# Performance work log

Hardware: AMD Instinct MI355X
Metric: run time of the kernel (lower is better)

Reference implementation:

```python
import jax, jax.numpy as jnp
import numpy as np

NA, NM = 200000, 100000
DA, DM = 128, 64
H = 128
E = 1000000


def _lin(x, W, b):
    # torch nn.Linear: y = x @ W.T + b, W: [out, in]
    return x @ W.T + b


def setup_inputs() -> dict:
    key = jax.random.key(0)
    ks = jax.random.split(key, 24)
    s = 0.02
    inp = {
        "x_account": jax.random.normal(ks[0], (NA, DA), jnp.float32),
        "x_merchant": jax.random.normal(ks[1], (NM, DM), jnp.float32),
        "e_am_src": jax.random.randint(ks[2], (E,), 0, NA, jnp.int32),
        "e_am_dst": jax.random.randint(ks[3], (E,), 0, NM, jnp.int32),
        "e_am_w": jax.random.uniform(ks[4], (E,), jnp.float32),
        "e_ma_src": jax.random.randint(ks[5], (E,), 0, NM, jnp.int32),
        "e_ma_dst": jax.random.randint(ks[6], (E,), 0, NA, jnp.int32),
        "e_ma_w": jax.random.uniform(ks[7], (E,), jnp.float32),
        # type_proj
        "Wp_a": s * jax.random.normal(ks[8], (H, DA), jnp.float32),
        "bp_a": jnp.zeros((H,), jnp.float32),
        "Wp_m": s * jax.random.normal(ks[9], (H, DM), jnp.float32),
        "bp_m": jnp.zeros((H,), jnp.float32),
        # rel_linears: account->merchant:txn (in=DA), merchant->account:rev (in=DM)
        "Wr_am": s * jax.random.normal(ks[10], (H, DA), jnp.float32),
        "br_am": jnp.zeros((H,), jnp.float32),
        "Wr_ma": s * jax.random.normal(ks[11], (H, DM), jnp.float32),
        "br_ma": jnp.zeros((H,), jnp.float32),
        # combine MLPs (Linear(2H,H) + ReLU)
        "Wc_a": s * jax.random.normal(ks[12], (H, 2 * H), jnp.float32),
        "bc_a": jnp.zeros((H,), jnp.float32),
        "Wc_m": s * jax.random.normal(ks[13], (H, 2 * H), jnp.float32),
        "bc_m": jnp.zeros((H,), jnp.float32),
        # account_out
        "Wo": s * jax.random.normal(ks[14], (1, H), jnp.float32),
        "bo": jnp.zeros((1,), jnp.float32),
    }
    return inp


def reference(x_account, x_merchant, e_am_src, e_am_dst, e_am_w,
              e_ma_src, e_ma_dst, e_ma_w,
              Wp_a, bp_a, Wp_m, bp_m,
              Wr_am, br_am, Wr_ma, br_ma,
              Wc_a, bc_a, Wc_m, bc_m, Wo, bo):
    # self projection per node type
    proj_a = _lin(x_account, Wp_a, bp_a)   # [NA, H]
    proj_m = _lin(x_merchant, Wp_m, bp_m)  # [NM, H]

    # relation account->merchant: lin(src feats) then SpMM (weighted scatter-add to dst)
    lin_am = _lin(x_account, Wr_am, br_am)                    # [NA, H]
    msg_am = e_am_w[:, None] * lin_am[e_am_src]               # [E, H]
    neigh_m = jax.ops.segment_sum(msg_am, e_am_dst, num_segments=proj_m.shape[0])

    # relation merchant->account
    lin_ma = _lin(x_merchant, Wr_ma, br_ma)                   # [NM, H]
    msg_ma = e_ma_w[:, None] * lin_ma[e_ma_src]               # [E, H]
    neigh_a = jax.ops.segment_sum(msg_ma, e_ma_dst, num_segments=proj_a.shape[0])

    # concat + MLP combine per node type
    h_a = jax.nn.relu(_lin(jnp.concatenate([proj_a, neigh_a], axis=1), Wc_a, bc_a))
    h_m = jax.nn.relu(_lin(jnp.concatenate([proj_m, neigh_m], axis=1), Wc_m, bc_m))
    _ = h_m  # computed in original but only account head is returned

    acct_out = jax.nn.sigmoid(_lin(h_a, Wo, bo))[:, 0]        # [NA]
    return acct_out
```

## Files before the change

### kernel.cpp

```cpp
#include <hip/hip_runtime.h>


typedef __attribute__((ext_vector_type(8))) short short8;
typedef __attribute__((ext_vector_type(4))) float f32x4;

#define PSH 12

__device__ inline unsigned short f32_bf16(float f) {
  unsigned int u = __float_as_uint(f);
  u += 0x7FFF + ((u >> 16) & 1);
  return (unsigned short)(u >> 16);
}
__device__ inline unsigned int pk_bf16(float a, float b) {
  return (unsigned int)f32_bf16(a) | ((unsigned int)f32_bf16(b) << 16);
}

__global__ __launch_bounds__(256) void setup_kernel(
    const float* __restrict__ xm, unsigned int* __restrict__ xmbf, int npairs,
    const int* __restrict__ dst, int* __restrict__ counts, int E,
    const float* __restrict__ Wp_a, const float* __restrict__ bp_a,
    const float* __restrict__ Wr_ma, const float* __restrict__ br_ma,
    const float* __restrict__ Wc_a, const float* __restrict__ bc_a,
    unsigned short* __restrict__ Wcomb, float* __restrict__ beff,
    float* __restrict__ vbr, int nb_cvt, int nb_hist) {
  __shared__ float wc_s[256];
  int b = blockIdx.x;
  int t = threadIdx.x;
  if (b < nb_cvt) {
    int i = b * 256 + t;
    if (i < npairs) {
      float2 v = ((const float2*)xm)[i];
      xmbf[i] = pk_bf16(v.x, v.y);
    }
    return;
  }
  b -= nb_cvt;
  if (b < nb_hist) {
    int e = b * 256 + t;
    if (e < E) atomicAdd(&counts[dst[e]], 1);
    return;
  }
  int col = b - nb_hist;
  wc_s[t] = Wc_a[col * 256 + t];
  __syncthreads();
  int wave = t >> 6, lane = t & 63;
  if (wave < 2) {
    int k = t;
    float acc = 0.f;
#pragma unroll
    for (int j = 0; j < 128; j += 4) {
      float a0 = Wp_a[(j + 0) * 128 + k];
      float a1 = Wp_a[(j + 1) * 128 + k];
      float a2 = Wp_a[(j + 2) * 128 + k];
      float a3 = Wp_a[(j + 3) * 128 + k];
      acc += wc_s[j] * a0 + wc_s[j + 1] * a1 + wc_s[j + 2] * a2 + wc_s[j + 3] * a3;
    }
    Wcomb[col * 192 + k] = f32_bf16(acc);
  } else if (wave == 2) {
    int kk = lane;
    float acc = 0.f;
#pragma unroll
    for (int j = 0; j < 128; j += 4) {
      float a0 = Wr_ma[(j + 0) * 64 + kk];
      float a1 = Wr_ma[(j + 1) * 64 + kk];
      float a2 = Wr_ma[(j + 2) * 64 + kk];
      float a3 = Wr_ma[(j + 3) * 64 + kk];
      acc += wc_s[128 + j] * a0 + wc_s[129 + j] * a1 + wc_s[130 + j] * a2 + wc_s[131 + j] * a3;
    }
    Wcomb[col * 192 + 128 + kk] = f32_bf16(acc);
  } else {
    float v1 = wc_s[lane] * bp_a[lane] + wc_s[lane + 64] * bp_a[lane + 64];
    float v2 = wc_s[128 + lane] * br_ma[lane] + wc_s[192 + lane] * br_ma[lane + 64];
#pragma unroll
    for (int m = 1; m <= 32; m <<= 1) {
      v1 += __shfl_xor(v1, m, 64);
      v2 += __shfl_xor(v2, m, 64);
    }
    if (lane == 0) { beff[col] = v1 + bc_a[col]; vbr[col] = v2; }
  }
}

__global__ void scan_a(const int* __restrict__ counts, int* __restrict__ bsum, int NA) {
  __shared__ int tmp[256];
  int t = threadIdx.x;
  int i = blockIdx.x * 256 + t;
  tmp[t] = (i < NA) ? counts[i] : 0;
  __syncthreads();
  for (int off = 128; off > 0; off >>= 1) {
    if (t < off) tmp[t] += tmp[t + off];
    __syncthreads();
  }
  if (t == 0) bsum[blockIdx.x] = tmp[0];
}

__global__ void scan_b(const int* __restrict__ bsum, int* __restrict__ bexcl, int nb) {
  __shared__ int tmp[1024];
  int t = threadIdx.x;
  int v = (t < nb) ? bsum[t] : 0;
  tmp[t] = v;
  __syncthreads();
  for (int off = 1; off < 1024; off <<= 1) {
    int x = (t >= off) ? tmp[t - off] : 0;
    __syncthreads();
    tmp[t] += x;
    __syncthreads();
  }
  bexcl[t] = tmp[t] - v;
}

__global__ void scan_c(const int* __restrict__ counts, const int* __restrict__ bexcl,
                       int* __restrict__ rowstart, int* __restrict__ cursor, int NA) {
  __shared__ int tmp[256];
  int t = threadIdx.x;
  int i = blockIdx.x * 256 + t;
  int v = (i < NA) ? counts[i] : 0;
  tmp[t] = v;
  __syncthreads();
  for (int off = 1; off < 256; off <<= 1) {
    int x = (t >= off) ? tmp[t - off] : 0;
    __syncthreads();
    tmp[t] += x;
    __syncthreads();
  }
  int excl = bexcl[blockIdx.x] + tmp[t] - v;
  if (i < NA) { rowstart[i] = excl; cursor[i] = excl; }
  else if (i == NA) { rowstart[NA] = excl; }
}

__global__ void scatter_kernel(const int* __restrict__ src, const int* __restrict__ dst,
                               const float* __restrict__ w, int* __restrict__ cursor,
                               unsigned int* __restrict__ edges, int E) {
  int slice = blockIdx.x >> 3;
  int p = blockIdx.x & 7;
  int e = slice * 256 + threadIdx.x;
  if (e >= E) return;
  int d = dst[e];
  if (((d >> PSH) & 7) != p) return;
  int pos = atomicAdd(&cursor[d], 1);
  unsigned int q = (unsigned int)fminf(w[e] * 32768.0f, 32767.0f);
  edges[pos] = (unsigned int)src[e] | (q << 17);
}

__global__ __launch_bounds__(256) void gather_kernel(
    const unsigned int* __restrict__ xmbf, const unsigned int* __restrict__ edges,
    const int* __restrict__ rowstart, unsigned int* __restrict__ neighbf,
    float* __restrict__ sumw, int NA) {
  int wave = threadIdx.x >> 6, lane = threadIdx.x & 63;
  int a = blockIdx.x * 4 + wave;
  if (a >= NA) return;
  int half = lane >> 5;
  int fp = lane & 31;
  int s0 = rowstart[a], s1 = rowstart[a + 1];
  float accx = 0.f, accy = 0.f, ws = 0.f;
  const float wscale = 1.0f / 32768.0f;
  for (int e0 = s0; e0 < s1; e0 += 8) {
#pragma unroll
    for (int k = 0; k < 4; ++k) {
      int e = e0 + k * 2 + half;
      bool valid = e < s1;
      unsigned int p = edges[valid ? e : s0];
      float w = valid ? (float)(p >> 17) * wscale : 0.f;
      unsigned int s = p & 0x1ffffu;
      unsigned int xp = xmbf[(size_t)s * 32 + fp];
      float x0 = __uint_as_float(xp << 16);
      float x1 = __uint_as_float(xp & 0xffff0000u);
      accx += w * x0;
      accy += w * x1;
      ws += w;
    }
  }
  accx += __shfl_xor(accx, 32, 64);
  accy += __shfl_xor(accy, 32, 64);
  ws   += __shfl_xor(ws, 32, 64);
  if (half == 0) {
    neighbf[(size_t)a * 32 + fp] = pk_bf16(accx, accy);
    if (fp == 0) sumw[a] = ws;
  }
}

__global__ __launch_bounds__(256) void acct_kernel(
    const float* __restrict__ xa, const unsigned int* __restrict__ neighbf,
    const float* __restrict__ sumw, const unsigned int* __restrict__ Wcomb32,
    const float* __restrict__ beff, const float* __restrict__ vbr,
    const float* __restrict__ Wo, const float* __restrict__ bo,
    float* __restrict__ out, int NA) {
  __shared__ unsigned int B_lds[24 * 128 * 4];
  int tid = threadIdx.x;
#pragma unroll
  for (int it = 0; it < 12; ++it) {
    int i = tid + it * 256;
    int c = i >> 7, col = i & 127;
    uint4 v = ((const uint4*)Wcomb32)[col * 24 + c];
    *((uint4*)&B_lds[i * 4]) = v;
  }
  __syncthreads();

  int wave = tid >> 6, lane = tid & 63;
  int n15 = lane & 15, quad = lane >> 4;
  float bo0 = bo[0];

  union U4 { uint4 u; short8 h; };

#pragma unroll
  for (int tile = 0; tile < 2; ++tile) {
    int rowbase = blockIdx.x * 128 + (wave * 2 + tile) * 16;
    int m = rowbase + n15;
    int mc = min(m, NA - 1);

    U4 afr[6];
    const float* xrow = xa + (size_t)mc * 128 + quad * 8;
#pragma unroll
    for (int s = 0; s < 4; ++s) {
      float4 f0 = ((const float4*)(xrow + s * 32))[0];
      float4 f1 = ((const float4*)(xrow + s * 32))[1];
      afr[s].u = make_uint4(pk_bf16(f0.x, f0.y), pk_bf16(f0.z, f0.w),
                            pk_bf16(f1.x, f1.y), pk_bf16(f1.z, f1.w));
    }
#pragma unroll
    for (int s = 0; s < 2; ++s) {
      afr[4 + s].u = ((const uint4*)(neighbf + (size_t)mc * 32))[s * 4 + quad];
    }

    f32x4 acc[8];
#pragma unroll
    for (int t = 0; t < 8; ++t) acc[t] = (f32x4){0.f, 0.f, 0.f, 0.f};

#pragma unroll
    for (int s = 0; s < 6; ++s) {
#pragma unroll
      for (int t = 0; t < 8; ++t) {
        U4 bfr;
        bfr.u = *((const uint4*)&B_lds[((s * 4 + quad) * 128 + t * 16 + n15) * 4]);
        acc[t] = __builtin_amdgcn_mfma_f32_16x16x32_bf16(afr[s].h, bfr.h, acc[t], 0, 0, 0);
      }
    }

    float sw[4];
#pragma unroll
    for (int r = 0; r < 4; ++r) {
      int grow = rowbase + quad * 4 + r;
      sw[r] = (grow < NA) ? sumw[grow] : 0.f;
    }
    float rowsum[4] = {0.f, 0.f, 0.f, 0.f};
#pragma unroll
    for (int t = 0; t < 8; ++t) {
      int col = t * 16 + n15;
      float be = beff[col], vb = vbr[col], wo = Wo[col];
#pragma unroll
      for (int r = 0; r < 4; ++r) {
        float h = acc[t][r] + be + sw[r] * vb;
        h = fmaxf(h, 0.f);
        rowsum[r] += h * wo;
      }
    }
#pragma unroll
    for (int msk = 1; msk <= 8; msk <<= 1) {
#pragma unroll
      for (int r = 0; r < 4; ++r) rowsum[r] += __shfl_xor(rowsum[r], msk, 64);
    }
    if (n15 == 0) {
#pragma unroll
      for (int r = 0; r < 4; ++r) {
        int grow = rowbase + quad * 4 + r;
        if (grow < NA) out[grow] = 1.0f / (1.0f + __expf(-(rowsum[r] + bo0)));
      }
    }
  }
}

extern "C" void kernel_launch(void* const* d_in, const int* in_sizes, int n_in,
                              void* d_out, int out_size, void* d_ws, size_t ws_size,
                              hipStream_t stream) {
  const float* xa      = (const float*)d_in[0];
  const float* xm      = (const float*)d_in[1];
  const int*   ema_src = (const int*)d_in[5];
  const int*   ema_dst = (const int*)d_in[6];
  const float* ema_w   = (const float*)d_in[7];
  const float* Wp_a    = (const float*)d_in[8];
  const float* bp_a    = (const float*)d_in[9];
  const float* Wr_ma   = (const float*)d_in[14];
  const float* br_ma   = (const float*)d_in[15];
  const float* Wc_a    = (const float*)d_in[16];
  const float* bc_a    = (const float*)d_in[17];
  const float* Wo      = (const float*)d_in[20];
  const float* bo      = (const float*)d_in[21];

  int NA = in_sizes[0] / 128;
  int NM = in_sizes[1] / 64;
  int E  = in_sizes[5];

  char* ws = (char*)d_ws;
  size_t off = 0;
  auto take = [&](size_t bytes) { char* p = ws + off; off = (off + bytes + 255) & ~(size_t)255; return p; };
  unsigned int* neighbf = (unsigned int*)take((size_t)NA * 32 * 4);
  unsigned int* xmbf    = (unsigned int*)take((size_t)NM * 32 * 4);
  float* sumw           = (float*)take((size_t)NA * 4);
  int* counts           = (int*)take((size_t)NA * 4);
  int* rowstart         = (int*)take((size_t)(NA + 1) * 4);
  int* cursor           = (int*)take((size_t)NA * 4);
  int* bsum             = (int*)take(1024 * 4);
  int* bexcl            = (int*)take(1024 * 4);
  unsigned int* edges   = (unsigned int*)take((size_t)E * 4);
  unsigned short* Wcomb = (unsigned short*)take(128 * 192 * 2);
  float* beff           = (float*)take(128 * 4);
  float* vbr            = (float*)take(128 * 4);

  hipMemsetAsync(counts, 0, (size_t)NA * 4, stream);

  int npairs = NM * 32;
  int nb_cvt = (npairs + 255) / 256;
  int nb_hist = (E + 255) / 256;
  setup_kernel<<<nb_cvt + nb_hist + 128, 256, 0, stream>>>(
      xm, xmbf, npairs, ema_dst, counts, E,
      Wp_a, bp_a, Wr_ma, br_ma, Wc_a, bc_a, Wcomb, beff, vbr, nb_cvt, nb_hist);

  int nb = (NA + 256) / 256;
  scan_a<<<nb, 256, 0, stream>>>(counts, bsum, NA);
  scan_b<<<1, 1024, 0, stream>>>(bsum, bexcl, nb);
  scan_c<<<nb, 256, 0, stream>>>(counts, bexcl, rowstart, cursor, NA);

  scatter_kernel<<<nb_hist * 8, 256, 0, stream>>>(ema_src, ema_dst, ema_w, cursor, edges, E);

  int gb = (NA + 3) / 4;
  gather_kernel<<<gb, 256, 0, stream>>>(xmbf, edges, rowstart, neighbf, sumw, NA);

  int ab = (NA + 127) / 128;
  acct_kernel<<<ab, 256, 0, stream>>>(xa, neighbf, sumw, (const unsigned int*)Wcomb,
                                      beff, vbr, Wo, bo, (float*)d_out, NA);
}
```

Before: 366.2 us.

## Fuse three-pass scan into decoupled look-back scan and widen gather loads

Replaces the three scan kernels with one single-pass scan that uses a ticket counter and a decoupled look-back over per-block status words, which removes two kernel launches and an extra pass over the counts array. The status and ticket buffers are zeroed by the same memset as counts. The gather kernel now has each lane load a uint2 (four bf16 features) and handles four edges per wave step instead of two, which adds one more shuffle reduction stage. The look-back spins serially on a single thread and relies on atomics for progress between blocks.

```diff
diff --git a/kernel.cpp b/kernel.cpp
--- a/kernel.cpp
+++ b/kernel.cpp
@@ -80,39 +80,17 @@
   }
 }
 
-__global__ void scan_a(const int* __restrict__ counts, int* __restrict__ bsum, int NA) {
+__global__ __launch_bounds__(256) void scan_kernel(
+    const int* __restrict__ counts, int* __restrict__ rowstart,
+    int* __restrict__ cursor, unsigned long long* __restrict__ status,
+    int* __restrict__ ticket, int NA) {
   __shared__ int tmp[256];
+  __shared__ int sh_bid, sh_prev;
   int t = threadIdx.x;
-  int i = blockIdx.x * 256 + t;
-  tmp[t] = (i < NA) ? counts[i] : 0;
-  __syncthreads();
-  for (int off = 128; off > 0; off >>= 1) {
-    if (t < off) tmp[t] += tmp[t + off];
-    __syncthreads();
-  }
-  if (t == 0) bsum[blockIdx.x] = tmp[0];
-}
-
-__global__ void scan_b(const int* __restrict__ bsum, int* __restrict__ bexcl, int nb) {
-  __shared__ int tmp[1024];
-  int t = threadIdx.x;
-  int v = (t < nb) ? bsum[t] : 0;
-  tmp[t] = v;
-  __syncthreads();
-  for (int off = 1; off < 1024; off <<= 1) {
-    int x = (t >= off) ? tmp[t - off] : 0;
-    __syncthreads();
-    tmp[t] += x;
-    __syncthreads();
-  }
-  bexcl[t] = tmp[t] - v;
-}
-
-__global__ void scan_c(const int* __restrict__ counts, const int* __restrict__ bexcl,
-                       int* __restrict__ rowstart, int* __restrict__ cursor, int NA) {
-  __shared__ int tmp[256];
-  int t = threadIdx.x;
-  int i = blockIdx.x * 256 + t;
+  if (t == 0) sh_bid = atomicAdd(ticket, 1);
+  __syncthreads();
+  int bid = sh_bid;
+  int i = bid * 256 + t;
   int v = (i < NA) ? counts[i] : 0;
   tmp[t] = v;
   __syncthreads();
@@ -122,7 +100,29 @@
     tmp[t] += x;
     __syncthreads();
   }
-  int excl = bexcl[blockIdx.x] + tmp[t] - v;
+  int incl = tmp[t];
+  int aggregate = tmp[255];
+  if (t == 0) {
+    if (bid == 0) {
+      atomicExch(&status[0], (2ULL << 32) | (unsigned int)aggregate);
+      sh_prev = 0;
+    } else {
+      atomicExch(&status[bid], (1ULL << 32) | (unsigned int)aggregate);
+      int prev = 0;
+      int j = bid - 1;
+      while (j >= 0) {
+        unsigned long long s;
+        do { s = atomicAdd(&status[j], 0ULL); } while ((s >> 32) == 0ULL);
+        prev += (int)(unsigned int)s;
+        if ((s >> 32) == 2ULL) break;
+        --j;
+      }
+      sh_prev = prev;
+      atomicExch(&status[bid], (2ULL << 32) | (unsigned int)(prev + aggregate));
+    }
+  }
+  __syncthreads();
+  int excl = sh_prev + incl - v;
   if (i < NA) { rowstart[i] = excl; cursor[i] = excl; }
   else if (i == NA) { rowstart[NA] = excl; }
 }
@@ -148,33 +148,39 @@
   int wave = threadIdx.x >> 6, lane = threadIdx.x & 63;
   int a = blockIdx.x * 4 + wave;
   if (a >= NA) return;
-  int half = lane >> 5;
-  int fp = lane & 31;
+  int q = lane >> 4;
+  int l = lane & 15;
   int s0 = rowstart[a], s1 = rowstart[a + 1];
-  float accx = 0.f, accy = 0.f, ws = 0.f;
+  float a0 = 0.f, a1 = 0.f, a2 = 0.f, a3 = 0.f, ws = 0.f;
   const float wscale = 1.0f / 32768.0f;
   for (int e0 = s0; e0 < s1; e0 += 8) {
 #pragma unroll
-    for (int k = 0; k < 4; ++k) {
-      int e = e0 + k * 2 + half;
+    for (int k = 0; k < 2; ++k) {
+      int e = e0 + k * 4 + q;
       bool valid = e < s1;
       unsigned int p = edges[valid ? e : s0];
       float w = valid ? (float)(p >> 17) * wscale : 0.f;
       unsigned int s = p & 0x1ffffu;
-      unsigned int xp = xmbf[(size_t)s * 32 + fp];
-      float x0 = __uint_as_float(xp << 16);
-      float x1 = __uint_as_float(xp & 0xffff0000u);
-      accx += w * x0;
-      accy += w * x1;
+      uint2 xp = ((const uint2*)(xmbf + (size_t)s * 32))[l];
+      a0 += w * __uint_as_float(xp.x << 16);
+      a1 += w * __uint_as_float(xp.x & 0xffff0000u);
+      a2 += w * __uint_as_float(xp.y << 16);
+      a3 += w * __uint_as_float(xp.y & 0xffff0000u);
       ws += w;
     }
   }
-  accx += __shfl_xor(accx, 32, 64);
-  accy += __shfl_xor(accy, 32, 64);
-  ws   += __shfl_xor(ws, 32, 64);
-  if (half == 0) {
-    neighbf[(size_t)a * 32 + fp] = pk_bf16(accx, accy);
-    if (fp == 0) sumw[a] = ws;
+  a0 += __shfl_xor(a0, 16, 64); a1 += __shfl_xor(a1, 16, 64);
+  a2 += __shfl_xor(a2, 16, 64); a3 += __shfl_xor(a3, 16, 64);
+  ws += __shfl_xor(ws, 16, 64);
+  a0 += __shfl_xor(a0, 32, 64); a1 += __shfl_xor(a1, 32, 64);
+  a2 += __shfl_xor(a2, 32, 64); a3 += __shfl_xor(a3, 32, 64);
+  ws += __shfl_xor(ws, 32, 64);
+  if (q == 0) {
+    uint2 o;
+    o.x = pk_bf16(a0, a1);
+    o.y = pk_bf16(a2, a3);
+    ((uint2*)(neighbf + (size_t)a * 32))[l] = o;
+    if (l == 0) sumw[a] = ws;
   }
 }
 
@@ -295,17 +301,20 @@
   unsigned int* neighbf = (unsigned int*)take((size_t)NA * 32 * 4);
   unsigned int* xmbf    = (unsigned int*)take((size_t)NM * 32 * 4);
   float* sumw           = (float*)take((size_t)NA * 4);
+  size_t zoff0 = off;
+  int nb_scan = (NA + 256) / 256;
   int* counts           = (int*)take((size_t)NA * 4);
+  unsigned long long* status = (unsigned long long*)take((size_t)nb_scan * 8);
+  int* ticket           = (int*)take(256);
+  size_t zlen = off - zoff0;
   int* rowstart         = (int*)take((size_t)(NA + 1) * 4);
   int* cursor           = (int*)take((size_t)NA * 4);
-  int* bsum             = (int*)take(1024 * 4);
-  int* bexcl            = (int*)take(1024 * 4);
   unsigned int* edges   = (unsigned int*)take((size_t)E * 4);
   unsigned short* Wcomb = (unsigned short*)take(128 * 192 * 2);
   float* beff           = (float*)take(128 * 4);
   float* vbr            = (float*)take(128 * 4);
 
-  hipMemsetAsync(counts, 0, (size_t)NA * 4, stream);
+  hipMemsetAsync(ws + zoff0, 0, zlen, stream);
 
   int npairs = NM * 32;
   int nb_cvt = (npairs + 255) / 256;
@@ -314,10 +323,7 @@
       xm, xmbf, npairs, ema_dst, counts, E,
       Wp_a, bp_a, Wr_ma, br_ma, Wc_a, bc_a, Wcomb, beff, vbr, nb_cvt, nb_hist);
 
-  int nb = (NA + 256) / 256;
-  scan_a<<<nb, 256, 0, stream>>>(counts, bsum, NA);
-  scan_b<<<1, 1024, 0, stream>>>(bsum, bexcl, nb);
-  scan_c<<<nb, 256, 0, stream>>>(counts, bexcl, rowstart, cursor, NA);
+  scan_kernel<<<nb_scan, 256, 0, stream>>>(counts, rowstart, cursor, status, ticket, NA);
 
   scatter_kernel<<<nb_hist * 8, 256, 0, stream>>>(ema_src, ema_dst, ema_w, cursor, edges, E);
 
```

After: 383.8 us. +4.8%, slower.
